# Performance work log

Hardware: AMD Instinct MI355X
Metric: run time of the kernel (lower is better)

## Reference

```python
import jax, jax.numpy as jnp
import numpy as np

N = 40000      # nodes
E = 640000     # edges (avg degree 16)
F = 128        # in_feats
OUT = 128      # out_feats


def setup_inputs() -> dict:
    key = jax.random.key(0)
    ks = jax.random.split(key, 8)
    feat = jax.random.normal(ks[0], (N, F), dtype=jnp.float32)
    src = jax.random.randint(ks[1], (E,), 0, N, dtype=jnp.int32)
    dst = jnp.sort(jax.random.randint(ks[2], (E,), 0, N, dtype=jnp.int32))
    # AttentionAGG: fc1 (2F -> F), fc2 (F -> 1); fc_layer (2F -> OUT)
    s1 = 1.0 / np.sqrt(2 * F)
    s2 = 1.0 / np.sqrt(F)
    w1 = jax.random.normal(ks[3], (2 * F, F), dtype=jnp.float32) * s1
    b1 = jnp.zeros((F,), dtype=jnp.float32)
    w2 = jax.random.normal(ks[4], (F, 1), dtype=jnp.float32) * s2
    b2 = jnp.zeros((1,), dtype=jnp.float32)
    wf = jax.random.normal(ks[5], (2 * F, OUT), dtype=jnp.float32) * s1
    bf = jnp.zeros((OUT,), dtype=jnp.float32)
    return {"feat": feat, "src": src, "dst": dst,
            "w1": w1, "b1": b1, "w2": w2, "b2": b2, "wf": wf, "bf": bf}


def reference(feat, src, dst, w1, b1, w2, b2, wf, bf):
    f = feat.shape[1]
    n = feat.shape[0]
    # fc1(concat(h_dst, m_src)) == h_dst @ w1[:F] + h_src @ w1[F:]  (edge_weight is None)
    proj_dst = feat @ w1[:f]          # [N, F]
    proj_src = feat @ w1[f:]          # [N, F]
    pre = jnp.tanh(proj_dst[dst] + proj_src[src] + b1)   # [E, F]
    scores = (pre @ w2)[:, 0] + b2[0]                    # [E]
    # softmax over the ragged incoming-edge set of each dst node
    smax = jax.ops.segment_max(scores, dst, num_segments=n, indices_are_sorted=True)
    ex = jnp.exp(scores - jax.lax.stop_gradient(smax)[dst])
    den = jax.ops.segment_sum(ex, dst, num_segments=n, indices_are_sorted=True)
    att = ex / den[dst]                                  # [E]
    # weighted segment-sum of messages (m_e = feat[src]); zero-degree nodes get 0
    neigh = jax.ops.segment_sum(att[:, None] * feat[src], dst,
                                num_segments=n, indices_are_sorted=True)  # [N, F]
    # fc_layer(concat(h_self, neigh))
    rst = feat @ wf[:f] + neigh @ wf[f:] + bf            # [N, OUT]
    return rst
```

## Files before the change

### kernel.cpp

```cpp
#include <hip/hip_runtime.h>
#include <math.h>

#define F 128
#define OUT 128

typedef unsigned short ushort_t;
typedef __attribute__((ext_vector_type(8))) short bfrag;
typedef __attribute__((ext_vector_type(4))) float ffrag;

__device__ __forceinline__ float bf_lo(unsigned int u) {
    return __uint_as_float(u << 16);
}
__device__ __forceinline__ float bf_hi(unsigned int u) {
    return __uint_as_float(u & 0xffff0000u);
}
__device__ __forceinline__ ushort_t f2bf(float f) {
    unsigned int x = __float_as_uint(f);
    unsigned int r = x + 0x7fffu + ((x >> 16) & 1u);
    return (ushort_t)(r >> 16);
}

__global__ __launch_bounds__(256) void cast_feat_kernel(
    const float* __restrict__ feat, ushort_t* __restrict__ abig,
    ushort_t* __restrict__ srcpack, int n)
{
    int i = blockIdx.x * 256 + threadIdx.x;
    if (i >= n * 16) return;
    int row = i >> 4, c = (i & 15) * 8;
    float4 a = *(const float4*)(feat + (size_t)row * F + c);
    float4 b = *(const float4*)(feat + (size_t)row * F + c + 4);
    ushort4 u0 = make_ushort4(f2bf(a.x), f2bf(a.y), f2bf(a.z), f2bf(a.w));
    ushort4 u1 = make_ushort4(f2bf(b.x), f2bf(b.y), f2bf(b.z), f2bf(b.w));
    *(ushort4*)(abig + (size_t)row * 256 + c) = u0;
    *(ushort4*)(abig + (size_t)row * 256 + c + 4) = u1;
    *(ushort4*)(srcpack + (size_t)row * 256 + c * 2 + 4) = u0;
    *(ushort4*)(srcpack + (size_t)row * 256 + c * 2 + 12) = u1;
}

__global__ __launch_bounds__(256) void cast_w_kernel(
    const float* __restrict__ w1, const float* __restrict__ wf,
    ushort_t* __restrict__ btp, ushort_t* __restrict__ btf)
{
    int i = blockIdx.x * 256 + threadIdx.x;
    if (i < 32768) {
        int j = i >> 7, k = i & 127;
        float v = (j < 128) ? w1[(size_t)k * F + j]
                            : w1[(size_t)(128 + k) * F + (j - 128)];
        btp[i] = f2bf(v);
    } else {
        int idx = i - 32768;
        int j = idx >> 8, k = idx & 255;
        btf[idx] = f2bf(wf[(size_t)k * F + j]);
    }
}

__global__ void rowptr_kernel(const int* __restrict__ dst,
                              int* __restrict__ row_ptr, int e, int n)
{
    int i = blockIdx.x * blockDim.x + threadIdx.x;
    if (i >= e) return;
    int d = dst[i];
    int prev = (i == 0) ? -1 : dst[i - 1];
    for (int v = prev + 1; v <= d; ++v) row_ptr[v] = i;
    if (i == e - 1) {
        for (int v = d + 1; v <= n; ++v) row_ptr[v] = e;
    }
}

#define PSTRIDE 136
__global__ __launch_bounds__(256) void proj_mfma_kernel(
    const ushort_t* __restrict__ abig, const ushort_t* __restrict__ btp,
    const float* __restrict__ b1, ushort_t* __restrict__ e_dst,
    ushort_t* __restrict__ srcpack, int n)
{
    __shared__ ushort_t As[64 * PSTRIDE];
    const int t = threadIdx.x;
    const int wv = t >> 6, lane = t & 63;
    const int lm = lane & 15, quad = lane >> 4;
    const int row0 = blockIdx.x * 64;
    const int col0 = wv * 64;

    for (int i = t; i < 1024; i += 256) {
        int r = i >> 4, c8 = (i & 15) * 8;
        uint4 d = make_uint4(0, 0, 0, 0);
        if (row0 + r < n)
            d = *(const uint4*)(abig + (size_t)(row0 + r) * 256 + c8);
        *(uint4*)(As + r * PSTRIDE + c8) = d;
    }
    __syncthreads();

    ffrag acc[4][4];
#pragma unroll
    for (int mi = 0; mi < 4; ++mi)
#pragma unroll
        for (int ni = 0; ni < 4; ++ni) acc[mi][ni] = (ffrag){0.f, 0.f, 0.f, 0.f};

#pragma unroll
    for (int ks = 0; ks < 4; ++ks) {
        bfrag bfr[4];
#pragma unroll
        for (int ni = 0; ni < 4; ++ni)
            bfr[ni] = *(const bfrag*)(btp + (size_t)(col0 + ni * 16 + lm) * 128
                                      + ks * 32 + quad * 8);
#pragma unroll
        for (int mi = 0; mi < 4; ++mi) {
            bfrag af = *(const bfrag*)(As + (mi * 16 + lm) * PSTRIDE
                                       + ks * 32 + quad * 8);
#pragma unroll
            for (int ni = 0; ni < 4; ++ni)
                acc[mi][ni] = __builtin_amdgcn_mfma_f32_16x16x32_bf16(
                    af, bfr[ni], acc[mi][ni], 0, 0, 0);
        }
    }

#pragma unroll
    for (int ni = 0; ni < 4; ++ni) {
        const int j = col0 + ni * 16 + lm;
        const float bias = (j < F) ? b1[j] : 0.f;
#pragma unroll
        for (int mi = 0; mi < 4; ++mi) {
#pragma unroll
            for (int r = 0; r < 4; ++r) {
                int row = row0 + mi * 16 + quad * 4 + r;
                if (row >= n) continue;
                ushort_t ub = f2bf(__expf(2.f * (acc[mi][ni][r] + bias)));
                if (j < F) {
                    e_dst[(size_t)row * F + j] = ub;
                } else {
                    int f = j - F;
                    srcpack[(size_t)row * 256 + (f >> 2) * 8 + (f & 3)] = ub;
                }
            }
        }
    }
}

__global__ __launch_bounds__(256) void fused_kernel(
    const ushort_t* __restrict__ e_dst, const ushort_t* __restrict__ srcpack,
    const int* __restrict__ src, const int* __restrict__ row_ptr,
    const float* __restrict__ w2, ushort_t* __restrict__ abig, int n)
{
    const int v = (int)((blockIdx.x * 256u + threadIdx.x) >> 5);
    const int fl = threadIdx.x & 31;
    const int sbase = threadIdx.x & 32;

    const float4 wv4 = ((const float4*)w2)[fl];
    const float w0 = wv4.x, w1_ = wv4.y, w2_ = wv4.z, w3_ = wv4.w;
    float sw = w0 + w1_ + w2_ + w3_;
    float aw = fabsf(w0) + fabsf(w1_) + fabsf(w2_) + fabsf(w3_);
#pragma unroll
    for (int off = 16; off; off >>= 1) {
        sw += __shfl_xor(sw, off, 64);
        aw += __shfl_xor(aw, off, 64);
    }
    const float K = sw - aw;

    if (v >= n) return;
    const int begin = row_ptr[v], end = row_ptr[v + 1];

    const uint2 ud = *(const uint2*)(e_dst + (size_t)v * F + fl * 4);
    const float ea0 = bf_lo(ud.x), ea1 = bf_hi(ud.x);
    const float ea2 = bf_lo(ud.y), ea3 = bf_hi(ud.y);

    float s = 0.f, a0 = 0.f, a1 = 0.f, a2 = 0.f, a3 = 0.f;

    for (int cb = begin; cb < end; cb += 32) {
        const int clen = min(32, end - cb);
        const int sv = (fl < clen) ? src[cb + fl] : 0;
        int jj = 0;
        for (; jj + 2 <= clen; jj += 2) {
            const int s0 = __shfl(sv, sbase + jj, 64);
            const int s1 = __shfl(sv, sbase + jj + 1, 64);
            const uint4 u0 = ((const uint4*)(srcpack + (size_t)s0 * 256))[fl];
            const uint4 u1 = ((const uint4*)(srcpack + (size_t)s1 * 256))[fl];
            float r, p0, p1;
            r = __builtin_amdgcn_rcpf(fmaf(ea0, bf_lo(u0.x), 1.f)); p0 = w0 * r;
            r = __builtin_amdgcn_rcpf(fmaf(ea1, bf_hi(u0.x), 1.f)); p0 = fmaf(w1_, r, p0);
            r = __builtin_amdgcn_rcpf(fmaf(ea2, bf_lo(u0.y), 1.f)); p0 = fmaf(w2_, r, p0);
            r = __builtin_amdgcn_rcpf(fmaf(ea3, bf_hi(u0.y), 1.f)); p0 = fmaf(w3_, r, p0);
            r = __builtin_amdgcn_rcpf(fmaf(ea0, bf_lo(u1.x), 1.f)); p1 = w0 * r;
            r = __builtin_amdgcn_rcpf(fmaf(ea1, bf_hi(u1.x), 1.f)); p1 = fmaf(w1_, r, p1);
            r = __builtin_amdgcn_rcpf(fmaf(ea2, bf_lo(u1.y), 1.f)); p1 = fmaf(w2_, r, p1);
            r = __builtin_amdgcn_rcpf(fmaf(ea3, bf_hi(u1.y), 1.f)); p1 = fmaf(w3_, r, p1);
#pragma unroll
            for (int off = 16; off; off >>= 1) {
                p0 += __shfl_xor(p0, off, 64);
                p1 += __shfl_xor(p1, off, 64);
            }
            const float g0 = __expf(fmaf(-2.f, p0, K));
            const float g1 = __expf(fmaf(-2.f, p1, K));
            s += g0 + g1;
            a0 = fmaf(g0, bf_lo(u0.z), fmaf(g1, bf_lo(u1.z), a0));
            a1 = fmaf(g0, bf_hi(u0.z), fmaf(g1, bf_hi(u1.z), a1));
            a2 = fmaf(g0, bf_lo(u0.w), fmaf(g1, bf_lo(u1.w), a2));
            a3 = fmaf(g0, bf_hi(u0.w), fmaf(g1, bf_hi(u1.w), a3));
        }
        if (jj < clen) {
            const int s0 = __shfl(sv, sbase + jj, 64);
            const uint4 u0 = ((const uint4*)(srcpack + (size_t)s0 * 256))[fl];
            float r, p0;
            r = __builtin_amdgcn_rcpf(fmaf(ea0, bf_lo(u0.x), 1.f)); p0 = w0 * r;
            r = __builtin_amdgcn_rcpf(fmaf(ea1, bf_hi(u0.x), 1.f)); p0 = fmaf(w1_, r, p0);
            r = __builtin_amdgcn_rcpf(fmaf(ea2, bf_lo(u0.y), 1.f)); p0 = fmaf(w2_, r, p0);
            r = __builtin_amdgcn_rcpf(fmaf(ea3, bf_hi(u0.y), 1.f)); p0 = fmaf(w3_, r, p0);
#pragma unroll
            for (int off = 16; off; off >>= 1) p0 += __shfl_xor(p0, off, 64);
            const float g0 = __expf(fmaf(-2.f, p0, K));
            s += g0;
            a0 = fmaf(g0, bf_lo(u0.z), a0);
            a1 = fmaf(g0, bf_hi(u0.z), a1);
            a2 = fmaf(g0, bf_lo(u0.w), a2);
            a3 = fmaf(g0, bf_hi(u0.w), a3);
        }
    }

    const float inv = (end > begin) ? 1.f / s : 0.f;
    ushort4 o = make_ushort4(f2bf(a0 * inv), f2bf(a1 * inv),
                             f2bf(a2 * inv), f2bf(a3 * inv));
    *(ushort4*)(abig + (size_t)v * 256 + 128 + fl * 4) = o;
}

#define OSTRIDE 264
__global__ __launch_bounds__(256) void out_mfma_kernel(
    const ushort_t* __restrict__ abig, const ushort_t* __restrict__ btf,
    const float* __restrict__ bfv, float* __restrict__ out, int n)
{
    __shared__ ushort_t As[64 * OSTRIDE];
    const int t = threadIdx.x;
    const int wv = t >> 6, lane = t & 63;
    const int lm = lane & 15, quad = lane >> 4;
    const int row0 = blockIdx.x * 64;
    const int col0 = wv * 32;

    for (int i = t; i < 2048; i += 256) {
        int r = i >> 5, c8 = (i & 31) * 8;
        uint4 d = make_uint4(0, 0, 0, 0);
        if (row0 + r < n)
            d = *(const uint4*)(abig + (size_t)(row0 + r) * 256 + c8);
        *(uint4*)(As + r * OSTRIDE + c8) = d;
    }
    __syncthreads();

    ffrag acc[4][2];
#pragma unroll
    for (int mi = 0; mi < 4; ++mi)
#pragma unroll
        for (int ni = 0; ni < 2; ++ni) acc[mi][ni] = (ffrag){0.f, 0.f, 0.f, 0.f};

#pragma unroll
    for (int ks = 0; ks < 8; ++ks) {
        bfrag bfr[2];
#pragma unroll
        for (int ni = 0; ni < 2; ++ni)
            bfr[ni] = *(const bfrag*)(btf + (size_t)(col0 + ni * 16 + lm) * 256
                                      + ks * 32 + quad * 8);
#pragma unroll
        for (int mi = 0; mi < 4; ++mi) {
            bfrag af = *(const bfrag*)(As + (mi * 16 + lm) * OSTRIDE
                                       + ks * 32 + quad * 8);
#pragma unroll
            for (int ni = 0; ni < 2; ++ni)
                acc[mi][ni] = __builtin_amdgcn_mfma_f32_16x16x32_bf16(
                    af, bfr[ni], acc[mi][ni], 0, 0, 0);
        }
    }

#pragma unroll
    for (int ni = 0; ni < 2; ++ni) {
        const int j = col0 + ni * 16 + lm;
        const float bb = bfv[j];
#pragma unroll
        for (int mi = 0; mi < 4; ++mi) {
#pragma unroll
            for (int r = 0; r < 4; ++r) {
                int row = row0 + mi * 16 + quad * 4 + r;
                if (row < n) out[(size_t)row * OUT + j] = acc[mi][ni][r] + bb;
            }
        }
    }
}

extern "C" void kernel_launch(void* const* d_in, const int* in_sizes, int n_in,
                              void* d_out, int out_size, void* d_ws, size_t ws_size,
                              hipStream_t stream)
{
    const float* feat = (const float*)d_in[0];
    const int*   src  = (const int*)d_in[1];
    const int*   dst  = (const int*)d_in[2];
    const float* w1   = (const float*)d_in[3];
    const float* b1   = (const float*)d_in[4];
    const float* w2   = (const float*)d_in[5];
    const float* b2   = (const float*)d_in[6];  (void)b2;
    const float* wf   = (const float*)d_in[7];
    const float* bfv  = (const float*)d_in[8];
    float* out = (float*)d_out;

    const int n = in_sizes[0] / F;
    const int e = in_sizes[1];

    ushort_t* abig    = (ushort_t*)d_ws;
    ushort_t* e_dst   = abig + (size_t)n * 256;
    ushort_t* srcpack = e_dst + (size_t)n * 128;
    ushort_t* btp     = srcpack + (size_t)n * 256;
    ushort_t* btf     = btp + 32768;
    int* row_ptr      = (int*)(btf + 32768);

    cast_feat_kernel<<<(n * 16 + 255) / 256, 256, 0, stream>>>(feat, abig, srcpack, n);
    cast_w_kernel<<<256, 256, 0, stream>>>(w1, wf, btp, btf);
    rowptr_kernel<<<(e + 255) / 256, 256, 0, stream>>>(dst, row_ptr, e, n);
    proj_mfma_kernel<<<(n + 63) / 64, 256, 0, stream>>>(abig, btp, b1, e_dst, srcpack, n);
    fused_kernel<<<(n + 7) / 8, 256, 0, stream>>>(e_dst, srcpack, src, row_ptr, w2, abig, n);
    out_mfma_kernel<<<(n + 63) / 64, 256, 0, stream>>>(abig, btf, bfv, out, n);
}
```

Before: 178.9 us.

## Fuse feature/weight casts and rowptr into projection kernel; unroll edge loop by four

Merges the feature cast, weight cast and row_ptr construction into one launch with the projection GEMM. Feature rows are converted to bf16 directly into shared memory and the workspace, weights are read as fp32 and packed into MFMA fragments on the fly, and extra blocks build row_ptr. This cuts three kernel launches and the separate cast passes. The cost is strided uncoalesced fp32 weight loads repeated in every GEMM block, in both the projection and output kernels. The edge aggregation loop also now handles four edges per iteration instead of two to expose more memory-level parallelism.

```diff
diff --git a/kernel.cpp b/kernel.cpp
--- a/kernel.cpp
+++ b/kernel.cpp
@@ -7,6 +7,8 @@
 typedef unsigned short ushort_t;
 typedef __attribute__((ext_vector_type(8))) short bfrag;
 typedef __attribute__((ext_vector_type(4))) float ffrag;
+
+union BU { unsigned u[4]; bfrag b; };
 
 __device__ __forceinline__ float bf_lo(unsigned int u) {
     return __uint_as_float(u << 16);
@@ -19,60 +21,30 @@
     unsigned int r = x + 0x7fffu + ((x >> 16) & 1u);
     return (ushort_t)(r >> 16);
 }
-
-__global__ __launch_bounds__(256) void cast_feat_kernel(
-    const float* __restrict__ feat, ushort_t* __restrict__ abig,
-    ushort_t* __restrict__ srcpack, int n)
+__device__ __forceinline__ unsigned pk2(float lo, float hi) {
+    return (unsigned)f2bf(lo) | ((unsigned)f2bf(hi) << 16);
+}
+
+#define PSTRIDE 136
+__global__ __launch_bounds__(256) void mega_kernel(
+    const float* __restrict__ feat, const float* __restrict__ w1,
+    const float* __restrict__ b1, const int* __restrict__ dst,
+    int* __restrict__ row_ptr, ushort_t* __restrict__ e_dst,
+    ushort_t* __restrict__ srcpack, ushort_t* __restrict__ abig,
+    int n, int e, int nproj)
 {
-    int i = blockIdx.x * 256 + threadIdx.x;
-    if (i >= n * 16) return;
-    int row = i >> 4, c = (i & 15) * 8;
-    float4 a = *(const float4*)(feat + (size_t)row * F + c);
-    float4 b = *(const float4*)(feat + (size_t)row * F + c + 4);
-    ushort4 u0 = make_ushort4(f2bf(a.x), f2bf(a.y), f2bf(a.z), f2bf(a.w));
-    ushort4 u1 = make_ushort4(f2bf(b.x), f2bf(b.y), f2bf(b.z), f2bf(b.w));
-    *(ushort4*)(abig + (size_t)row * 256 + c) = u0;
-    *(ushort4*)(abig + (size_t)row * 256 + c + 4) = u1;
-    *(ushort4*)(srcpack + (size_t)row * 256 + c * 2 + 4) = u0;
-    *(ushort4*)(srcpack + (size_t)row * 256 + c * 2 + 12) = u1;
-}
-
-__global__ __launch_bounds__(256) void cast_w_kernel(
-    const float* __restrict__ w1, const float* __restrict__ wf,
-    ushort_t* __restrict__ btp, ushort_t* __restrict__ btf)
-{
-    int i = blockIdx.x * 256 + threadIdx.x;
-    if (i < 32768) {
-        int j = i >> 7, k = i & 127;
-        float v = (j < 128) ? w1[(size_t)k * F + j]
-                            : w1[(size_t)(128 + k) * F + (j - 128)];
-        btp[i] = f2bf(v);
-    } else {
-        int idx = i - 32768;
-        int j = idx >> 8, k = idx & 255;
-        btf[idx] = f2bf(wf[(size_t)k * F + j]);
-    }
-}
-
-__global__ void rowptr_kernel(const int* __restrict__ dst,
-                              int* __restrict__ row_ptr, int e, int n)
-{
-    int i = blockIdx.x * blockDim.x + threadIdx.x;
-    if (i >= e) return;
-    int d = dst[i];
-    int prev = (i == 0) ? -1 : dst[i - 1];
-    for (int v = prev + 1; v <= d; ++v) row_ptr[v] = i;
-    if (i == e - 1) {
-        for (int v = d + 1; v <= n; ++v) row_ptr[v] = e;
-    }
-}
-
-#define PSTRIDE 136
-__global__ __launch_bounds__(256) void proj_mfma_kernel(
-    const ushort_t* __restrict__ abig, const ushort_t* __restrict__ btp,
-    const float* __restrict__ b1, ushort_t* __restrict__ e_dst,
-    ushort_t* __restrict__ srcpack, int n)
-{
+    if ((int)blockIdx.x >= nproj) {
+        int i = ((int)blockIdx.x - nproj) * 256 + threadIdx.x;
+        if (i >= e) return;
+        int d = dst[i];
+        int prev = (i == 0) ? -1 : dst[i - 1];
+        for (int v = prev + 1; v <= d; ++v) row_ptr[v] = i;
+        if (i == e - 1) {
+            for (int v = d + 1; v <= n; ++v) row_ptr[v] = e;
+        }
+        return;
+    }
+
     __shared__ ushort_t As[64 * PSTRIDE];
     const int t = threadIdx.x;
     const int wv = t >> 6, lane = t & 63;
@@ -80,12 +52,36 @@
     const int row0 = blockIdx.x * 64;
     const int col0 = wv * 64;
 
-    for (int i = t; i < 1024; i += 256) {
-        int r = i >> 4, c8 = (i & 15) * 8;
-        uint4 d = make_uint4(0, 0, 0, 0);
-        if (row0 + r < n)
-            d = *(const uint4*)(abig + (size_t)(row0 + r) * 256 + c8);
-        *(uint4*)(As + r * PSTRIDE + c8) = d;
+    {
+        const int r = t >> 2, q = t & 3;
+        const int row = row0 + r;
+        unsigned up[16];
+        if (row < n) {
+            const float* fp = feat + (size_t)row * F + 32 * q;
+#pragma unroll
+            for (int i4 = 0; i4 < 8; ++i4) {
+                float4 a = *(const float4*)(fp + 4 * i4);
+                up[2 * i4]     = pk2(a.x, a.y);
+                up[2 * i4 + 1] = pk2(a.z, a.w);
+            }
+        } else {
+#pragma unroll
+            for (int i2 = 0; i2 < 16; ++i2) up[i2] = 0;
+        }
+#pragma unroll
+        for (int i4 = 0; i4 < 4; ++i4)
+            *(uint4*)(As + r * PSTRIDE + 32 * q + 8 * i4) =
+                make_uint4(up[4 * i4], up[4 * i4 + 1], up[4 * i4 + 2], up[4 * i4 + 3]);
+        if (row < n) {
+#pragma unroll
+            for (int i4 = 0; i4 < 4; ++i4)
+                *(uint4*)(abig + (size_t)row * 256 + 32 * q + 8 * i4) =
+                    make_uint4(up[4 * i4], up[4 * i4 + 1], up[4 * i4 + 2], up[4 * i4 + 3]);
+#pragma unroll
+            for (int i4 = 0; i4 < 8; ++i4)
+                *(uint2*)(srcpack + (size_t)row * 256 + (8 * q + i4) * 8 + 4) =
+                    make_uint2(up[2 * i4], up[2 * i4 + 1]);
+        }
     }
     __syncthreads();
 
@@ -99,9 +95,19 @@
     for (int ks = 0; ks < 4; ++ks) {
         bfrag bfr[4];
 #pragma unroll
-        for (int ni = 0; ni < 4; ++ni)
-            bfr[ni] = *(const bfrag*)(btp + (size_t)(col0 + ni * 16 + lm) * 128
-                                      + ks * 32 + quad * 8);
+        for (int ni = 0; ni < 4; ++ni) {
+            const int jj = col0 + ni * 16 + lm;
+            const float* wcol = (jj < F) ? (w1 + jj) : (w1 + (size_t)F * F + (jj - F));
+            const int k0 = ks * 32 + quad * 8;
+            BU bu;
+#pragma unroll
+            for (int l = 0; l < 4; ++l) {
+                float x0 = wcol[(size_t)(k0 + 2 * l) * F];
+                float x1 = wcol[(size_t)(k0 + 2 * l + 1) * F];
+                bu.u[l] = pk2(x0, x1);
+            }
+            bfr[ni] = bu.b;
+        }
 #pragma unroll
         for (int mi = 0; mi < 4; ++mi) {
             bfrag af = *(const bfrag*)(As + (mi * 16 + lm) * PSTRIDE
@@ -168,34 +174,40 @@
         const int clen = min(32, end - cb);
         const int sv = (fl < clen) ? src[cb + fl] : 0;
         int jj = 0;
-        for (; jj + 2 <= clen; jj += 2) {
-            const int s0 = __shfl(sv, sbase + jj, 64);
-            const int s1 = __shfl(sv, sbase + jj + 1, 64);
-            const uint4 u0 = ((const uint4*)(srcpack + (size_t)s0 * 256))[fl];
-            const uint4 u1 = ((const uint4*)(srcpack + (size_t)s1 * 256))[fl];
-            float r, p0, p1;
-            r = __builtin_amdgcn_rcpf(fmaf(ea0, bf_lo(u0.x), 1.f)); p0 = w0 * r;
-            r = __builtin_amdgcn_rcpf(fmaf(ea1, bf_hi(u0.x), 1.f)); p0 = fmaf(w1_, r, p0);
-            r = __builtin_amdgcn_rcpf(fmaf(ea2, bf_lo(u0.y), 1.f)); p0 = fmaf(w2_, r, p0);
-            r = __builtin_amdgcn_rcpf(fmaf(ea3, bf_hi(u0.y), 1.f)); p0 = fmaf(w3_, r, p0);
-            r = __builtin_amdgcn_rcpf(fmaf(ea0, bf_lo(u1.x), 1.f)); p1 = w0 * r;
-            r = __builtin_amdgcn_rcpf(fmaf(ea1, bf_hi(u1.x), 1.f)); p1 = fmaf(w1_, r, p1);
-            r = __builtin_amdgcn_rcpf(fmaf(ea2, bf_lo(u1.y), 1.f)); p1 = fmaf(w2_, r, p1);
-            r = __builtin_amdgcn_rcpf(fmaf(ea3, bf_hi(u1.y), 1.f)); p1 = fmaf(w3_, r, p1);
+        for (; jj + 4 <= clen; jj += 4) {
+            uint4 u[4];
+#pragma unroll
+            for (int q = 0; q < 4; ++q) {
+                const int sq = __shfl(sv, sbase + jj + q, 64);
+                u[q] = ((const uint4*)(srcpack + (size_t)sq * 256))[fl];
+            }
+            float p[4];
+#pragma unroll
+            for (int q = 0; q < 4; ++q) {
+                float r;
+                r = __builtin_amdgcn_rcpf(fmaf(ea0, bf_lo(u[q].x), 1.f)); p[q] = w0 * r;
+                r = __builtin_amdgcn_rcpf(fmaf(ea1, bf_hi(u[q].x), 1.f)); p[q] = fmaf(w1_, r, p[q]);
+                r = __builtin_amdgcn_rcpf(fmaf(ea2, bf_lo(u[q].y), 1.f)); p[q] = fmaf(w2_, r, p[q]);
+                r = __builtin_amdgcn_rcpf(fmaf(ea3, bf_hi(u[q].y), 1.f)); p[q] = fmaf(w3_, r, p[q]);
+            }
 #pragma unroll
             for (int off = 16; off; off >>= 1) {
-                p0 += __shfl_xor(p0, off, 64);
-                p1 += __shfl_xor(p1, off, 64);
-            }
-            const float g0 = __expf(fmaf(-2.f, p0, K));
-            const float g1 = __expf(fmaf(-2.f, p1, K));
-            s += g0 + g1;
-            a0 = fmaf(g0, bf_lo(u0.z), fmaf(g1, bf_lo(u1.z), a0));
-            a1 = fmaf(g0, bf_hi(u0.z), fmaf(g1, bf_hi(u1.z), a1));
-            a2 = fmaf(g0, bf_lo(u0.w), fmaf(g1, bf_lo(u1.w), a2));
-            a3 = fmaf(g0, bf_hi(u0.w), fmaf(g1, bf_hi(u1.w), a3));
-        }
-        if (jj < clen) {
+#pragma unroll
+                for (int q = 0; q < 4; ++q) p[q] += __shfl_xor(p[q], off, 64);
+            }
+            float g[4];
+#pragma unroll
+            for (int q = 0; q < 4; ++q) g[q] = __expf(fmaf(-2.f, p[q], K));
+            s += (g[0] + g[1]) + (g[2] + g[3]);
+#pragma unroll
+            for (int q = 0; q < 4; ++q) {
+                a0 = fmaf(g[q], bf_lo(u[q].z), a0);
+                a1 = fmaf(g[q], bf_hi(u[q].z), a1);
+                a2 = fmaf(g[q], bf_lo(u[q].w), a2);
+                a3 = fmaf(g[q], bf_hi(u[q].w), a3);
+            }
+        }
+        for (; jj < clen; ++jj) {
             const int s0 = __shfl(sv, sbase + jj, 64);
             const uint4 u0 = ((const uint4*)(srcpack + (size_t)s0 * 256))[fl];
             float r, p0;
@@ -222,7 +234,7 @@
 
 #define OSTRIDE 264
 __global__ __launch_bounds__(256) void out_mfma_kernel(
-    const ushort_t* __restrict__ abig, const ushort_t* __restrict__ btf,
+    const ushort_t* __restrict__ abig, const float* __restrict__ wf,
     const float* __restrict__ bfv, float* __restrict__ out, int n)
 {
     __shared__ ushort_t As[64 * OSTRIDE];
@@ -251,9 +263,18 @@
     for (int ks = 0; ks < 8; ++ks) {
         bfrag bfr[2];
 #pragma unroll
-        for (int ni = 0; ni < 2; ++ni)
-            bfr[ni] = *(const bfrag*)(btf + (size_t)(col0 + ni * 16 + lm) * 256
-                                      + ks * 32 + quad * 8);
+        for (int ni = 0; ni < 2; ++ni) {
+            const int jj = col0 + ni * 16 + lm;
+            const int k0 = ks * 32 + quad * 8;
+            BU bu;
+#pragma unroll
+            for (int l = 0; l < 4; ++l) {
+                float x0 = wf[(size_t)(k0 + 2 * l) * F + jj];
+                float x1 = wf[(size_t)(k0 + 2 * l + 1) * F + jj];
+                bu.u[l] = pk2(x0, x1);
+            }
+            bfr[ni] = bu.b;
+        }
 #pragma unroll
         for (int mi = 0; mi < 4; ++mi) {
             bfrag af = *(const bfrag*)(As + (mi * 16 + lm) * OSTRIDE
@@ -301,14 +322,14 @@
     ushort_t* abig    = (ushort_t*)d_ws;
     ushort_t* e_dst   = abig + (size_t)n * 256;
     ushort_t* srcpack = e_dst + (size_t)n * 128;
-    ushort_t* btp     = srcpack + (size_t)n * 256;
-    ushort_t* btf     = btp + 32768;
-    int* row_ptr      = (int*)(btf + 32768);
-
-    cast_feat_kernel<<<(n * 16 + 255) / 256, 256, 0, stream>>>(feat, abig, srcpack, n);
-    cast_w_kernel<<<256, 256, 0, stream>>>(w1, wf, btp, btf);
-    rowptr_kernel<<<(e + 255) / 256, 256, 0, stream>>>(dst, row_ptr, e, n);
-    proj_mfma_kernel<<<(n + 63) / 64, 256, 0, stream>>>(abig, btp, b1, e_dst, srcpack, n);
-    fused_kernel<<<(n + 7) / 8, 256, 0, stream>>>(e_dst, srcpack, src, row_ptr, w2, abig, n);
-    out_mfma_kernel<<<(n + 63) / 64, 256, 0, stream>>>(abig, btf, bfv, out, n);
-}
+    int* row_ptr      = (int*)(srcpack + (size_t)n * 256);
+
+    const int nproj = (n + 63) / 64;
+    const int nrp   = (e + 255) / 256;
+
+    mega_kernel<<<nproj + nrp, 256, 0, stream>>>(
+        feat, w1, b1, dst, row_ptr, e_dst, srcpack, abig, n, e, nproj);
+    fused_kernel<<<(n + 7) / 8, 256, 0, stream>>>(
+        e_dst, srcpack, src, row_ptr, w2, abig, n);
+    out_mfma_kernel<<<(n + 63) / 64, 256, 0, stream>>>(abig, wf, bfv, out, n);
+}
```

Result: no change. 177.7 us (-0.6%).
